# Kernel tuning notes

Hardware: AMD Instinct MI355X
Metric: run time of the kernel (lower is better)

Reference implementation:

```python
import jax, jax.numpy as jnp
import numpy as np

N_SRC = 50000
N_EDGES = 150000
D_IN = 512
D_OUT = 512

def setup_inputs() -> dict:
    key = jax.random.key(0)
    k1, k2, k3, k4, k5 = jax.random.split(key, 5)
    src_h = jax.random.normal(k1, (N_SRC, D_IN), dtype=jnp.float32)
    W = jax.random.normal(k2, (D_OUT, D_IN), dtype=jnp.float32) * (1.0 / np.sqrt(D_IN))
    b = jax.random.normal(k3, (D_OUT,), dtype=jnp.float32) * 0.01
    src_idx = jax.random.randint(k4, (N_EDGES,), 0, N_SRC, dtype=jnp.int64) if jax.config.jax_enable_x64 else jax.random.randint(k4, (N_EDGES,), 0, N_SRC, dtype=jnp.int32)
    dst_idx = jax.random.randint(k5, (N_EDGES,), 0, N_SRC, dtype=src_idx.dtype)
    return {"src_h": src_h, "W": W, "b": b, "src_idx": src_idx, "dst_idx": dst_idx, "n_dst": N_SRC}

def reference(src_h, W, b, src_idx, dst_idx, n_dst):
    # message passing: copy src feature to each edge, sum into dst nodes
    msgs = src_h[src_idx]                                  # [E, D_in]
    agg = jax.ops.segment_sum(msgs, dst_idx, num_segments=n_dst)  # [N_dst, D_in]
    # dense linear (apply_linear == 'linear' -> no relu)
    return agg @ W.T + b                                   # [N_dst, D_out]
```

## Files before the change

kernel.cpp:

```cpp
#include <hip/hip_runtime.h>
#include <hip/hip_bf16.h>

#define D 512
#define BM 128
#define BN 128
#define BK 64
#define SB 512

typedef __attribute__((ext_vector_type(8))) short bf16x8;
typedef __attribute__((ext_vector_type(4))) float f32x4;

__device__ __forceinline__ unsigned short bf16_rne(float f) {
    union { float f; unsigned u; } v; v.f = f;
    return (unsigned short)((v.u + 0x7FFFu + ((v.u >> 16) & 1u)) >> 16);
}

__device__ __forceinline__ void gload16(const void* g, void* l) {
    __builtin_amdgcn_global_load_lds(
        (const __attribute__((address_space(1))) void*)g,
        (__attribute__((address_space(3))) void*)l,
        16, 0, 0);
}

__device__ __forceinline__ void facc(float4& a, const float4 v) {
    a.x += v.x; a.y += v.y; a.z += v.z; a.w += v.w;
}

__global__ __launch_bounds__(256) void prep_kernel(const float* __restrict__ W,
                                                   unsigned short* __restrict__ wb,
                                                   const int* __restrict__ dst, int E,
                                                   int* __restrict__ cnt) {
    const int b = blockIdx.x;
    const int t = threadIdx.x;
    if (b < 512) {
        const int i = b * 256 + t;
        float2 v = ((const float2*)W)[i];
        unsigned r = ((unsigned)bf16_rne(v.x)) | (((unsigned)bf16_rne(v.y)) << 16);
        ((unsigned*)wb)[i] = r;
    } else {
        const int e = (b - 512) * 256 + t;
        if (e < E) atomicAdd(&cnt[dst[e]], 1);
    }
}


__global__ __launch_bounds__(256) void scan_reduce_kernel(const int* __restrict__ cnt, int M,
                                                          int* __restrict__ bsum) {
    const int t = threadIdx.x;
    const int i0 = blockIdx.x * SB + t * 2;
    int v = 0;
    if (i0 < M)     v += cnt[i0];
    if (i0 + 1 < M) v += cnt[i0 + 1];
    #pragma unroll
    for (int o = 32; o > 0; o >>= 1) v += __shfl_down(v, o, 64);
    __shared__ int ws_[4];
    if ((t & 63) == 0) ws_[t >> 6] = v;
    __syncthreads();
    if (t == 0) bsum[blockIdx.x] = ws_[0] + ws_[1] + ws_[2] + ws_[3];
}

__global__ __launch_bounds__(256) void scan_final_kernel(int* __restrict__ cnt, int M,
                                                         const int* __restrict__ bsum, int NB,
                                                         int* __restrict__ offsets) {
    __shared__ int sb[256];
    __shared__ int s[256];
    const int t = threadIdx.x;

    int bv = (t < NB) ? bsum[t] : 0;
    sb[t] = bv;
    __syncthreads();
    #pragma unroll
    for (int o = 1; o < 256; o <<= 1) {
        int u = (t >= o) ? sb[t - o] : 0;
        __syncthreads();
        sb[t] += u;
        __syncthreads();
    }
    if (blockIdx.x == 0 && t == 255) offsets[M] = sb[255];
    const int bexcl = (blockIdx.x > 0) ? sb[blockIdx.x - 1] : 0;

    const int base = blockIdx.x * SB + t * 2;
    int a = (base < M) ? cnt[base] : 0;
    int b = (base + 1 < M) ? cnt[base + 1] : 0;
    const int tsum = a + b;
    s[t] = tsum;
    __syncthreads();
    #pragma unroll
    for (int o = 1; o < 256; o <<= 1) {
        int u = (t >= o) ? s[t - o] : 0;
        __syncthreads();
        s[t] += u;
        __syncthreads();
    }
    const int excl = s[t] - tsum + bexcl;
    if (base < M)     { offsets[base] = excl;         cnt[base] = excl; }
    if (base + 1 < M) { offsets[base + 1] = excl + a; cnt[base + 1] = excl + a; }
}

__global__ __launch_bounds__(256) void sort_kernel(const int* __restrict__ src,
                                                   const int* __restrict__ dst, int E,
                                                   int* __restrict__ cursor,
                                                   int* __restrict__ sorted_src) {
    int e = blockIdx.x * 256 + threadIdx.x;
    if (e < E) {
        int pos = atomicAdd(&cursor[dst[e]], 1);
        sorted_src[pos] = src[e];
    }
}

__global__ __launch_bounds__(256) void agg_kernel(const float* __restrict__ src_h,
                                                  const int* __restrict__ offsets,
                                                  const int* __restrict__ sorted_src,
                                                  unsigned short* __restrict__ aggb,
                                                  int M) {
    const int wv = threadIdx.x >> 6;
    const int lane = threadIdx.x & 63;
    const int d = blockIdx.x * 4 + wv;
    if (d >= M) return;
    const int beg = offsets[d];
    const int end = offsets[d + 1];
    const float4* rb = (const float4*)src_h;

    float4 a0 = {0.f, 0.f, 0.f, 0.f};
    float4 a1 = {0.f, 0.f, 0.f, 0.f};
    int e = beg;

    for (; e + 4 <= end; e += 4) {
        const int s0 = sorted_src[e];
        const int s1 = sorted_src[e + 1];
        const int s2 = sorted_src[e + 2];
        const int s3 = sorted_src[e + 3];
        float4 v00 = rb[(size_t)s0 * 128 + lane];
        float4 v01 = rb[(size_t)s0 * 128 + 64 + lane];
        float4 v10 = rb[(size_t)s1 * 128 + lane];
        float4 v11 = rb[(size_t)s1 * 128 + 64 + lane];
        float4 v20 = rb[(size_t)s2 * 128 + lane];
        float4 v21 = rb[(size_t)s2 * 128 + 64 + lane];
        float4 v30 = rb[(size_t)s3 * 128 + lane];
        float4 v31 = rb[(size_t)s3 * 128 + 64 + lane];
        facc(a0, v00); facc(a1, v01);
        facc(a0, v10); facc(a1, v11);
        facc(a0, v20); facc(a1, v21);
        facc(a0, v30); facc(a1, v31);
    }
    if (e + 2 <= end) {
        const int s0 = sorted_src[e];
        const int s1 = sorted_src[e + 1];
        float4 v00 = rb[(size_t)s0 * 128 + lane];
        float4 v01 = rb[(size_t)s0 * 128 + 64 + lane];
        float4 v10 = rb[(size_t)s1 * 128 + lane];
        float4 v11 = rb[(size_t)s1 * 128 + 64 + lane];
        facc(a0, v00); facc(a1, v01);
        facc(a0, v10); facc(a1, v11);
        e += 2;
    }
    if (e < end) {
        const int s0 = sorted_src[e];
        float4 v00 = rb[(size_t)s0 * 128 + lane];
        float4 v01 = rb[(size_t)s0 * 128 + 64 + lane];
        facc(a0, v00); facc(a1, v01);
    }

    ushort4 o0, o1;
    o0.x = bf16_rne(a0.x); o0.y = bf16_rne(a0.y);
    o0.z = bf16_rne(a0.z); o0.w = bf16_rne(a0.w);
    o1.x = bf16_rne(a1.x); o1.y = bf16_rne(a1.y);
    o1.z = bf16_rne(a1.z); o1.w = bf16_rne(a1.w);
    *(ushort4*)(aggb + (size_t)d * D + lane * 4) = o0;
    *(ushort4*)(aggb + (size_t)d * D + 256 + lane * 4) = o1;
}

__global__ __launch_bounds__(256) void gemm_kernel(const unsigned short* __restrict__ A,
                                                   const unsigned short* __restrict__ B,
                                                   const float* __restrict__ bias,
                                                   float* __restrict__ out,
                                                   int M, int MB_tiles) {
    __shared__ __align__(16) unsigned short As[BM * BK];
    __shared__ __align__(16) unsigned short Bs[BN * BK];

    const int L = blockIdx.x;
    const int mb = (L >> 5) * 8 + (L & 7);
    const int nb = (L >> 3) & 3;
    if (mb >= MB_tiles) return;
    const int m0 = mb * BM;
    const int n0 = nb * BN;

    const int t = threadIdx.x;
    const int lane = t & 63;
    const int wave = t >> 6;
    const int wm = wave >> 1;
    const int wn = wave & 1;
    const int quad = lane >> 4;
    const int lr = lane & 15;

    const int srow = t >> 3;
    const int scol = ((t & 7) ^ (srow & 7)) * 8;
    int arow[4], brow[4];
    #pragma unroll
    for (int q = 0; q < 4; ++q) {
        arow[q] = min(m0 + q * 32 + srow, M - 1);
        brow[q] = n0 + q * 32 + srow;
    }

    const int fs0 = (quad ^ (lr & 7)) * 8;

    f32x4 acc[4][4] = {};

    for (int k0 = 0; k0 < D; k0 += BK) {
        #pragma unroll
        for (int q = 0; q < 4; ++q) {
            gload16(A + (size_t)arow[q] * D + k0 + scol, As + q * 2048 + t * 8);
            gload16(B + (size_t)brow[q] * D + k0 + scol, Bs + q * 2048 + t * 8);
        }
        __syncthreads();

        #pragma unroll
        for (int kk = 0; kk < 2; ++kk) {
            const int fs = fs0 ^ (kk << 5);
            bf16x8 af[4], bfr[4];
            #pragma unroll
            for (int i = 0; i < 4; ++i) {
                af[i]  = *(const bf16x8*)&As[(wm * 64 + i * 16 + lr) * BK + fs];
                bfr[i] = *(const bf16x8*)&Bs[(wn * 64 + i * 16 + lr) * BK + fs];
            }
            #pragma unroll
            for (int i = 0; i < 4; ++i)
                #pragma unroll
                for (int j = 0; j < 4; ++j)
                    acc[i][j] = __builtin_amdgcn_mfma_f32_16x16x32_bf16(af[i], bfr[j], acc[i][j], 0, 0, 0);
        }
        __syncthreads();
    }

    #pragma unroll
    for (int j = 0; j < 4; ++j) {
        const int col = n0 + wn * 64 + j * 16 + lr;
        const float bv = bias[col];
        #pragma unroll
        for (int i = 0; i < 4; ++i) {
            const int rbase = m0 + wm * 64 + i * 16 + quad * 4;
            #pragma unroll
            for (int r = 0; r < 4; ++r) {
                const int row = rbase + r;
                if (row < M) out[(size_t)row * D + col] = acc[i][j][r] + bv;
            }
        }
    }
}

extern "C" void kernel_launch(void* const* d_in, const int* in_sizes, int n_in,
                              void* d_out, int out_size, void* d_ws, size_t ws_size,
                              hipStream_t stream) {
    const float* src_h = (const float*)d_in[0];
    const float* W     = (const float*)d_in[1];
    const float* b     = (const float*)d_in[2];
    const int*   si    = (const int*)d_in[3];
    const int*   di    = (const int*)d_in[4];
    const int M = in_sizes[0] / D;
    const int E = in_sizes[3];
    const int NB = (M + SB - 1) / SB;

    char* ws = (char*)d_ws;
    unsigned short* aggb = (unsigned short*)ws;
    unsigned short* wb   = (unsigned short*)(ws + 51200000);
    int* offsets         = (int*)(ws + 51724288);
    int* cnt             = (int*)(ws + 51924480);
    int* ssrc            = (int*)(ws + 52124480);
    int* bsum            = (int*)(ws + 52724480);

    hipMemsetAsync(cnt, 0, (size_t)M * sizeof(int), stream);
    const int HB = (E + 255) / 256;
    prep_kernel<<<dim3(512 + HB), 256, 0, stream>>>(W, wb, di, E, cnt);
    scan_reduce_kernel<<<dim3(NB), 256, 0, stream>>>(cnt, M, bsum);
    scan_final_kernel<<<dim3(NB), 256, 0, stream>>>(cnt, M, bsum, NB, offsets);
    sort_kernel<<<dim3((E + 255) / 256), 256, 0, stream>>>(si, di, E, cnt, ssrc);
    agg_kernel<<<dim3((M + 3) / 4), 256, 0, stream>>>(src_h, offsets, ssrc, aggb, M);

    const int MB_tiles = (M + BM - 1) / BM;
    const int ngrid = ((MB_tiles + 7) / 8) * 32;
    gemm_kernel<<<dim3(ngrid), 256, 0, stream>>>(aggb, wb, b, (float*)d_out, M, MB_tiles);
}
```

Measured before the change: 313.5 us.

## Double-buffer GEMM LDS tiles with BK=32 and vectorized float4 epilogue

Restructures the bf16 GEMM main loop to use two LDS buffers with a smaller K-tile, prefetching the next tile via global_load_lds while MFMAs run on the current one, and using a single barrier per iteration. It also swaps MFMA operand order so each lane holds four consecutive output columns, allowing float4 bias loads and float4 stores in the epilogue. This aims to hide global load latency and cut scattered scalar stores, at the cost of more loop iterations and a changed LDS swizzle.

```diff
diff --git a/kernel.cpp b/kernel.cpp
--- a/kernel.cpp
+++ b/kernel.cpp
@@ -4,7 +4,7 @@
 #define D 512
 #define BM 128
 #define BN 128
-#define BK 64
+#define BK 32
 #define SB 512
 
 typedef __attribute__((ext_vector_type(8))) short bf16x8;
@@ -175,8 +175,8 @@
                                                    const float* __restrict__ bias,
                                                    float* __restrict__ out,
                                                    int M, int MB_tiles) {
-    __shared__ __align__(16) unsigned short As[BM * BK];
-    __shared__ __align__(16) unsigned short Bs[BN * BK];
+    __shared__ __align__(16) unsigned short As[2 * BM * BK];
+    __shared__ __align__(16) unsigned short Bs[2 * BN * BK];
 
     const int L = blockIdx.x;
     const int mb = (L >> 5) * 8 + (L & 7);
@@ -193,57 +193,71 @@
     const int quad = lane >> 4;
     const int lr = lane & 15;
 
-    const int srow = t >> 3;
-    const int scol = ((t & 7) ^ (srow & 7)) * 8;
-    int arow[4], brow[4];
-    #pragma unroll
-    for (int q = 0; q < 4; ++q) {
-        arow[q] = min(m0 + q * 32 + srow, M - 1);
-        brow[q] = n0 + q * 32 + srow;
-    }
-
-    const int fs0 = (quad ^ (lr & 7)) * 8;
+    const int srow = t >> 2;
+    const int scol = ((t & 3) ^ ((t >> 3) & 3)) * 8;
+    const int arow0 = min(m0 + srow, M - 1);
+    const int arow1 = min(m0 + 64 + srow, M - 1);
+    const int brow0 = n0 + srow;
+    const int brow1 = n0 + 64 + srow;
+    const unsigned short* ag0 = A + (size_t)arow0 * D + scol;
+    const unsigned short* ag1 = A + (size_t)arow1 * D + scol;
+    const unsigned short* bg0 = B + (size_t)brow0 * D + scol;
+    const unsigned short* bg1 = B + (size_t)brow1 * D + scol;
+
+    const int fsw = (quad ^ ((lr >> 1) & 3)) * 8;
 
     f32x4 acc[4][4] = {};
 
-    for (int k0 = 0; k0 < D; k0 += BK) {
-        #pragma unroll
-        for (int q = 0; q < 4; ++q) {
-            gload16(A + (size_t)arow[q] * D + k0 + scol, As + q * 2048 + t * 8);
-            gload16(B + (size_t)brow[q] * D + k0 + scol, Bs + q * 2048 + t * 8);
-        }
-        __syncthreads();
-
-        #pragma unroll
-        for (int kk = 0; kk < 2; ++kk) {
-            const int fs = fs0 ^ (kk << 5);
-            bf16x8 af[4], bfr[4];
-            #pragma unroll
-            for (int i = 0; i < 4; ++i) {
-                af[i]  = *(const bf16x8*)&As[(wm * 64 + i * 16 + lr) * BK + fs];
-                bfr[i] = *(const bf16x8*)&Bs[(wn * 64 + i * 16 + lr) * BK + fs];
-            }
-            #pragma unroll
-            for (int i = 0; i < 4; ++i)
-                #pragma unroll
-                for (int j = 0; j < 4; ++j)
-                    acc[i][j] = __builtin_amdgcn_mfma_f32_16x16x32_bf16(af[i], bfr[j], acc[i][j], 0, 0, 0);
-        }
-        __syncthreads();
-    }
-
-    #pragma unroll
-    for (int j = 0; j < 4; ++j) {
-        const int col = n0 + wn * 64 + j * 16 + lr;
-        const float bv = bias[col];
+    gload16(ag0, As + t * 8);
+    gload16(ag1, As + 2048 + t * 8);
+    gload16(bg0, Bs + t * 8);
+    gload16(bg1, Bs + 2048 + t * 8);
+    asm volatile("s_waitcnt vmcnt(0)" ::: "memory");
+    __builtin_amdgcn_s_barrier();
+
+    for (int kt = 0; kt < 16; ++kt) {
+        const int cur = (kt & 1) * 4096;
+        const int nxt = 4096 - cur;
+        if (kt + 1 < 16) {
+            const int k0n = (kt + 1) * BK;
+            gload16(ag0 + k0n, As + nxt + t * 8);
+            gload16(ag1 + k0n, As + nxt + 2048 + t * 8);
+            gload16(bg0 + k0n, Bs + nxt + t * 8);
+            gload16(bg1 + k0n, Bs + nxt + 2048 + t * 8);
+        }
+
+        bf16x8 af[4], bfr[4];
         #pragma unroll
         for (int i = 0; i < 4; ++i) {
-            const int rbase = m0 + wm * 64 + i * 16 + quad * 4;
+            af[i]  = *(const bf16x8*)&As[cur + (wm * 64 + i * 16 + lr) * BK + fsw];
+            bfr[i] = *(const bf16x8*)&Bs[cur + (wn * 64 + i * 16 + lr) * BK + fsw];
+        }
+        #pragma unroll
+        for (int i = 0; i < 4; ++i)
             #pragma unroll
-            for (int r = 0; r < 4; ++r) {
-                const int row = rbase + r;
-                if (row < M) out[(size_t)row * D + col] = acc[i][j][r] + bv;
-            }
+            for (int j = 0; j < 4; ++j)
+                acc[i][j] = __builtin_amdgcn_mfma_f32_16x16x32_bf16(bfr[j], af[i], acc[i][j], 0, 0, 0);
+
+        if (kt + 1 < 16) {
+            asm volatile("s_waitcnt vmcnt(0)" ::: "memory");
+            __builtin_amdgcn_s_barrier();
+        }
+    }
+
+    #pragma unroll
+    for (int i = 0; i < 4; ++i) {
+        const int row = m0 + wm * 64 + i * 16 + lr;
+        if (row >= M) continue;
+        #pragma unroll
+        for (int j = 0; j < 4; ++j) {
+            const int colb = n0 + wn * 64 + j * 16 + quad * 4;
+            const float4 bv = *(const float4*)(bias + colb);
+            float4 o;
+            o.x = acc[i][j][0] + bv.x;
+            o.y = acc[i][j][1] + bv.y;
+            o.z = acc[i][j][2] + bv.z;
+            o.w = acc[i][j][3] + bv.w;
+            *(float4*)(out + (size_t)row * D + colb) = o;
         }
     }
 }
```

Measured after the change: 274.6 us. 1.14x faster.
